# Kernel tuning notes

Hardware: AMD Instinct MI355X
Metric: run time of the kernel (lower is better)

The kernel has to match this reference:

```python
import jax, jax.numpy as jnp
import numpy as np

B, H, W = 8, 1024, 1024
DIM = 33  # LUT resolution per axis


def identity_lut(dim=DIM):
    # lut[0, b, g, r] = r/(dim-1); lut[1, b, g, r] = g/(dim-1); lut[2, b, g, r] = b/(dim-1)
    coords = jnp.arange(dim, dtype=jnp.float32) / (dim - 1)
    r = jnp.broadcast_to(coords[None, None, :], (dim, dim, dim))
    g = jnp.broadcast_to(coords[None, :, None], (dim, dim, dim))
    b = jnp.broadcast_to(coords[:, None, None], (dim, dim, dim))
    return jnp.stack([r, g, b], axis=0)  # [3, dim, dim, dim]


def setup_inputs() -> dict:
    key = jax.random.key(0)
    x = jax.random.uniform(key, (B, 3, H, W), dtype=jnp.float32)  # RGB in [0,1)
    lut = identity_lut(DIM)  # learned parameter, identity init as in the module
    return {"lut": lut, "x": x}


def _trilinear_lut_apply(lut, x):
    # lut: [3, dim, dim, dim] indexed as [channel, b, g, r]; x: [B, 3, H, W] in [0,1]
    dim = lut.shape[1]
    scale = jnp.float32(dim - 1)
    r = x[:, 0] * scale  # [B, H, W]
    g = x[:, 1] * scale
    b = x[:, 2] * scale

    ir = jnp.clip(jnp.floor(r).astype(jnp.int32), 0, dim - 2)
    ig = jnp.clip(jnp.floor(g).astype(jnp.int32), 0, dim - 2)
    ib = jnp.clip(jnp.floor(b).astype(jnp.int32), 0, dim - 2)

    fr = r - ir.astype(x.dtype)
    fg = g - ig.astype(x.dtype)
    fb = b - ib.astype(x.dtype)

    lut_flat = lut.reshape(3, dim * dim * dim)  # [3, dim^3]
    base = (ib * dim + ig) * dim + ir  # flat index of (b,g,r) corner, [B,H,W]

    out = jnp.zeros_like(x)  # [B, 3, H, W]
    for db in (0, 1):
        wb = fb if db else (1.0 - fb)
        for dg in (0, 1):
            wg = fg if dg else (1.0 - fg)
            for dr in (0, 1):
                wr = fr if dr else (1.0 - fr)
                idx = base + (db * dim + dg) * dim + dr  # [B,H,W]
                corner = lut_flat[:, idx]  # gather -> [3, B, H, W]
                w = (wb * wg * wr)[None]  # [1, B, H, W]
                out = out + jnp.transpose(corner * w, (1, 0, 2, 3))
    return out


def reference(lut, x):
    return _trilinear_lut_apply(lut, x)
```

## Files before the change

### kernel.cpp

```cpp
#include <hip/hip_runtime.h>
#include <math.h>

typedef float        f32x4 __attribute__((ext_vector_type(4)));
typedef unsigned int u32x4 __attribute__((ext_vector_type(4)));

static constexpr int DIM    = 33;
static constexpr int LUT_N  = DIM * DIM * DIM;
static constexpr int HW     = 1024 * 1024;
static constexpr int BATCH  = 8;
static constexpr long NPIX  = (long)BATCH * HW;
static constexpr long NTASK = NPIX / 4;

static constexpr size_t QT_BYTES  = (size_t)LUT_N * 4;
static constexpr size_t LDS_BYTES = 143872;

static constexpr int ABLK = 256;
static constexpr int ATHR = 1024;

__device__ __forceinline__ f32x4 ntl4(const float* p) {
    return __builtin_nontemporal_load((const f32x4*)p);
}
__device__ __forceinline__ void nts4(float* p, f32x4 v) {
    __builtin_nontemporal_store(v, (f32x4*)p);
}
__device__ __forceinline__ float d_r(unsigned n) { return (float)(n & 1023u); }
__device__ __forceinline__ float d_g(unsigned n) { return (float)((n >> 10) & 1023u); }
__device__ __forceinline__ float d_b(unsigned n) { return (float)(n >> 20); }

__global__ __launch_bounds__(1024) void lut_fused(
    const float* __restrict__ x, const float* __restrict__ lut,
    float* __restrict__ out) {
    extern __shared__ unsigned sl[];
    const int t = threadIdx.x;

    float vmin = 1e30f, vmax = -1e30f;
    {
        const f32x4* l4 = (const f32x4*)lut;
        const int NV = (3 * LUT_N) / 4;
#pragma unroll 4
        for (int i = t; i < NV; i += 1024) {
            f32x4 v = l4[i];
            vmin = fminf(vmin, fminf(fminf(v[0], v[1]), fminf(v[2], v[3])));
            vmax = fmaxf(vmax, fmaxf(fmaxf(v[0], v[1]), fmaxf(v[2], v[3])));
        }
        if (t < 3) {
            float v = lut[NV * 4 + t];
            vmin = fminf(vmin, v);
            vmax = fmaxf(vmax, v);
        }
    }
#pragma unroll
    for (int off = 32; off > 0; off >>= 1) {
        vmin = fminf(vmin, __shfl_down(vmin, off));
        vmax = fmaxf(vmax, __shfl_down(vmax, off));
    }
    float* sf = (float*)sl;
    if ((t & 63) == 0) { sf[t >> 6] = vmin; sf[16 + (t >> 6)] = vmax; }
    __syncthreads();
    float mn = sf[0], mx = sf[16];
#pragma unroll
    for (int k = 1; k < 16; ++k) {
        mn = fminf(mn, sf[k]);
        mx = fmaxf(mx, sf[16 + k]);
    }
    __syncthreads();

    float range = mx - mn;
    if (range < 1e-20f) range = 1e-20f;
    const float qscale = 1023.0f / range;
    const float inv    = range * (1.0f / 1023.0f);

    for (int i = t; i < LUT_N; i += 1024) {
        float r = lut[i], g = lut[LUT_N + i], b = lut[2 * LUT_N + i];
        unsigned qr = (unsigned)__float2int_rn((r - mn) * qscale);
        unsigned qg = (unsigned)__float2int_rn((g - mn) * qscale);
        unsigned qb = (unsigned)__float2int_rn((b - mn) * qscale);
        sl[i] = qr | (qg << 10) | (qb << 20);
    }
    __syncthreads();

    const int gtid = blockIdx.x * ATHR + t;
    const size_t hw4 = (size_t)gtid * 4;
    const float* xp = x + hw4;
    float*       op = out + hw4;

    f32x4 rc = ntl4(xp);
    f32x4 gc = ntl4(xp + HW);
    f32x4 bc = ntl4(xp + 2 * (size_t)HW);

    for (int it = 0; it < BATCH; ++it) {
        f32x4 rn = {}, gn = {}, bn = {};
        if (it != BATCH - 1) {
            const float* xn = xp + (size_t)(it + 1) * (3 * (size_t)HW);
            rn = ntl4(xn);
            gn = ntl4(xn + HW);
            bn = ntl4(xn + 2 * (size_t)HW);
        }

        unsigned n[4][8];
        float fr[4], fg[4], fb[4];
#pragma unroll
        for (int i = 0; i < 4; ++i) {
            const float scale = (float)(DIM - 1);
            float rs = rc[i] * scale, gs = gc[i] * scale, bs = bc[i] * scale;
            int ir = (int)rs; ir = ir < 0 ? 0 : (ir > DIM - 2 ? DIM - 2 : ir);
            int ig = (int)gs; ig = ig < 0 ? 0 : (ig > DIM - 2 ? DIM - 2 : ig);
            int ib = (int)bs; ib = ib < 0 ? 0 : (ib > DIM - 2 ? DIM - 2 : ib);
            fr[i] = rs - (float)ir;
            fg[i] = gs - (float)ig;
            fb[i] = bs - (float)ib;
            int s = ib * (DIM * DIM) + ig * DIM + ir;
            n[i][0] = sl[s];                     n[i][1] = sl[s + 1];
            n[i][2] = sl[s + DIM];               n[i][3] = sl[s + DIM + 1];
            n[i][4] = sl[s + DIM * DIM];         n[i][5] = sl[s + DIM * DIM + 1];
            n[i][6] = sl[s + DIM * DIM + DIM];   n[i][7] = sl[s + DIM * DIM + DIM + 1];
        }

        f32x4 orv, ogv, obv;
#pragma unroll
        for (int i = 0; i < 4; ++i) {
            float frc = 1.0f - fr[i], fgc = 1.0f - fg[i], fbc = 1.0f - fb[i];
            float w00 = fbc * fgc, w01 = fbc * fg[i];
            float w10 = fb[i] * fgc, w11 = fb[i] * fg[i];
            float u0 = w00 * frc, u1 = w00 * fr[i];
            float u2 = w01 * frc, u3 = w01 * fr[i];
            float u4 = w10 * frc, u5 = w10 * fr[i];
            float u6 = w11 * frc, u7 = w11 * fr[i];

            float qr = u0 * d_r(n[i][0]);
            qr = fmaf(u1, d_r(n[i][1]), qr);
            qr = fmaf(u2, d_r(n[i][2]), qr);
            qr = fmaf(u3, d_r(n[i][3]), qr);
            qr = fmaf(u4, d_r(n[i][4]), qr);
            qr = fmaf(u5, d_r(n[i][5]), qr);
            qr = fmaf(u6, d_r(n[i][6]), qr);
            qr = fmaf(u7, d_r(n[i][7]), qr);

            float qg = u0 * d_g(n[i][0]);
            qg = fmaf(u1, d_g(n[i][1]), qg);
            qg = fmaf(u2, d_g(n[i][2]), qg);
            qg = fmaf(u3, d_g(n[i][3]), qg);
            qg = fmaf(u4, d_g(n[i][4]), qg);
            qg = fmaf(u5, d_g(n[i][5]), qg);
            qg = fmaf(u6, d_g(n[i][6]), qg);
            qg = fmaf(u7, d_g(n[i][7]), qg);

            float qb = u0 * d_b(n[i][0]);
            qb = fmaf(u1, d_b(n[i][1]), qb);
            qb = fmaf(u2, d_b(n[i][2]), qb);
            qb = fmaf(u3, d_b(n[i][3]), qb);
            qb = fmaf(u4, d_b(n[i][4]), qb);
            qb = fmaf(u5, d_b(n[i][5]), qb);
            qb = fmaf(u6, d_b(n[i][6]), qb);
            qb = fmaf(u7, d_b(n[i][7]), qb);

            orv[i] = fmaf(qr, inv, mn);
            ogv[i] = fmaf(qg, inv, mn);
            obv[i] = fmaf(qb, inv, mn);
        }

        float* o = op + (size_t)it * (3 * (size_t)HW);
        nts4(o, orv);
        nts4(o + HW, ogv);
        nts4(o + 2 * (size_t)HW, obv);

        rc = rn; gc = gn; bc = bn;
    }
}

__global__ __launch_bounds__(256) void lut_apply_soa(
    const float* __restrict__ x, const float* __restrict__ lut,
    float* __restrict__ out) {
    long t = (long)blockIdx.x * 256 + threadIdx.x;
    long p = t * 4;
    int  b  = (int)(p >> 20);
    int  hw = (int)(p & (HW - 1));
    size_t base = (size_t)b * (3 * (size_t)HW) + (size_t)hw;

    float4 rv = *(const float4*)(x + base);
    float4 gv = *(const float4*)(x + base + (size_t)HW);
    float4 bv = *(const float4*)(x + base + 2 * (size_t)HW);

    float rr[4] = {rv.x, rv.y, rv.z, rv.w};
    float gg[4] = {gv.x, gv.y, gv.z, gv.w};
    float bb[4] = {bv.x, bv.y, bv.z, bv.w};
    float orr[4], org[4], orb[4];

#pragma unroll
    for (int i = 0; i < 4; ++i) {
        const float scale = (float)(DIM - 1);
        float rs = rr[i] * scale, gs = gg[i] * scale, bs = bb[i] * scale;
        int ir = (int)floorf(rs); ir = ir < 0 ? 0 : (ir > DIM - 2 ? DIM - 2 : ir);
        int ig = (int)floorf(gs); ig = ig < 0 ? 0 : (ig > DIM - 2 ? DIM - 2 : ig);
        int ib = (int)floorf(bs); ib = ib < 0 ? 0 : (ib > DIM - 2 ? DIM - 2 : ib);
        float fr = rs - (float)ir, fg = gs - (float)ig, fb = bs - (float)ib;
        int base_i = (ib * DIM + ig) * DIM + ir;
        float acc[3] = {0.f, 0.f, 0.f};
#pragma unroll
        for (int db = 0; db < 2; ++db) {
            float wb = db ? fb : 1.f - fb;
#pragma unroll
            for (int dg = 0; dg < 2; ++dg) {
                float wg = dg ? fg : 1.f - fg;
#pragma unroll
                for (int dr = 0; dr < 2; ++dr) {
                    float wr = dr ? fr : 1.f - fr;
                    int idx = base_i + (db * DIM + dg) * DIM + dr;
                    float w = wb * wg * wr;
                    acc[0] = fmaf(w, lut[idx], acc[0]);
                    acc[1] = fmaf(w, lut[LUT_N + idx], acc[1]);
                    acc[2] = fmaf(w, lut[2 * LUT_N + idx], acc[2]);
                }
            }
        }
        orr[i] = acc[0]; org[i] = acc[1]; orb[i] = acc[2];
    }

    *(float4*)(out + base)                  = make_float4(orr[0], orr[1], orr[2], orr[3]);
    *(float4*)(out + base + (size_t)HW)     = make_float4(org[0], org[1], org[2], org[3]);
    *(float4*)(out + base + 2 * (size_t)HW) = make_float4(orb[0], orb[1], orb[2], orb[3]);
}

extern "C" void kernel_launch(void* const* d_in, const int* in_sizes, int n_in,
                              void* d_out, int out_size, void* d_ws, size_t ws_size,
                              hipStream_t stream) {
    const float* lut = (const float*)d_in[0];
    const float* x   = (const float*)d_in[1];
    if (n_in >= 2 && in_sizes[0] > in_sizes[1]) {
        lut = (const float*)d_in[1];
        x   = (const float*)d_in[0];
    }
    float* out = (float*)d_out;
    (void)d_ws; (void)ws_size;

    (void)hipFuncSetAttribute((const void*)lut_fused,
                              hipFuncAttributeMaxDynamicSharedMemorySize,
                              (int)LDS_BYTES);
    lut_fused<<<ABLK, ATHR, LDS_BYTES, stream>>>(x, lut, out);
}
```

Baseline: 188.6 us.

## Software-pipeline LUT gathers and prefetch inputs two batches ahead

```diff
diff --git a/kernel.cpp b/kernel.cpp
--- a/kernel.cpp
+++ b/kernel.cpp
@@ -11,7 +11,6 @@
 static constexpr long NPIX  = (long)BATCH * HW;
 static constexpr long NTASK = NPIX / 4;
 
-static constexpr size_t QT_BYTES  = (size_t)LUT_N * 4;
 static constexpr size_t LDS_BYTES = 143872;
 
 static constexpr int ABLK = 256;
@@ -26,12 +25,104 @@
 __device__ __forceinline__ float d_r(unsigned n) { return (float)(n & 1023u); }
 __device__ __forceinline__ float d_g(unsigned n) { return (float)((n >> 10) & 1023u); }
 __device__ __forceinline__ float d_b(unsigned n) { return (float)(n >> 20); }
+
+struct GS {
+    unsigned n[4][8];
+    float fr[4], fg[4], fb[4];
+};
+
+__device__ __forceinline__ void make_gather(const unsigned* __restrict__ sl,
+                                            f32x4 rc, f32x4 gc, f32x4 bc,
+                                            GS& g) {
+#pragma unroll
+    for (int i = 0; i < 4; ++i) {
+        const float scale = (float)(DIM - 1);
+        float rs = rc[i] * scale, gs = gc[i] * scale, bs = bc[i] * scale;
+        int ir = (int)rs; ir = ir < 0 ? 0 : (ir > DIM - 2 ? DIM - 2 : ir);
+        int ig = (int)gs; ig = ig < 0 ? 0 : (ig > DIM - 2 ? DIM - 2 : ig);
+        int ib = (int)bs; ib = ib < 0 ? 0 : (ib > DIM - 2 ? DIM - 2 : ib);
+        g.fr[i] = rs - (float)ir;
+        g.fg[i] = gs - (float)ig;
+        g.fb[i] = bs - (float)ib;
+        int s = ib * (DIM * DIM) + ig * DIM + ir;
+        g.n[i][0] = sl[s];                     g.n[i][1] = sl[s + 1];
+        g.n[i][2] = sl[s + DIM];               g.n[i][3] = sl[s + DIM + 1];
+        g.n[i][4] = sl[s + DIM * DIM];         g.n[i][5] = sl[s + DIM * DIM + 1];
+        g.n[i][6] = sl[s + DIM * DIM + DIM];   g.n[i][7] = sl[s + DIM * DIM + DIM + 1];
+    }
+}
+
+__device__ __forceinline__ void finish_store(const GS& g, float* __restrict__ o,
+                                             float inv, float mn) {
+    f32x4 orv, ogv, obv;
+#pragma unroll
+    for (int i = 0; i < 4; ++i) {
+        float fr = g.fr[i], fg = g.fg[i], fb = g.fb[i];
+        float frc = 1.0f - fr, fgc = 1.0f - fg, fbc = 1.0f - fb;
+        float w00 = fbc * fgc, w01 = fbc * fg;
+        float w10 = fb * fgc,  w11 = fb * fg;
+        float u0 = w00 * frc, u1 = w00 * fr;
+        float u2 = w01 * frc, u3 = w01 * fr;
+        float u4 = w10 * frc, u5 = w10 * fr;
+        float u6 = w11 * frc, u7 = w11 * fr;
+
+        float qr = u0 * d_r(g.n[i][0]);
+        qr = fmaf(u1, d_r(g.n[i][1]), qr);
+        qr = fmaf(u2, d_r(g.n[i][2]), qr);
+        qr = fmaf(u3, d_r(g.n[i][3]), qr);
+        qr = fmaf(u4, d_r(g.n[i][4]), qr);
+        qr = fmaf(u5, d_r(g.n[i][5]), qr);
+        qr = fmaf(u6, d_r(g.n[i][6]), qr);
+        qr = fmaf(u7, d_r(g.n[i][7]), qr);
+
+        float qg = u0 * d_g(g.n[i][0]);
+        qg = fmaf(u1, d_g(g.n[i][1]), qg);
+        qg = fmaf(u2, d_g(g.n[i][2]), qg);
+        qg = fmaf(u3, d_g(g.n[i][3]), qg);
+        qg = fmaf(u4, d_g(g.n[i][4]), qg);
+        qg = fmaf(u5, d_g(g.n[i][5]), qg);
+        qg = fmaf(u6, d_g(g.n[i][6]), qg);
+        qg = fmaf(u7, d_g(g.n[i][7]), qg);
+
+        float qb = u0 * d_b(g.n[i][0]);
+        qb = fmaf(u1, d_b(g.n[i][1]), qb);
+        qb = fmaf(u2, d_b(g.n[i][2]), qb);
+        qb = fmaf(u3, d_b(g.n[i][3]), qb);
+        qb = fmaf(u4, d_b(g.n[i][4]), qb);
+        qb = fmaf(u5, d_b(g.n[i][5]), qb);
+        qb = fmaf(u6, d_b(g.n[i][6]), qb);
+        qb = fmaf(u7, d_b(g.n[i][7]), qb);
+
+        orv[i] = fmaf(qr, inv, mn);
+        ogv[i] = fmaf(qg, inv, mn);
+        obv[i] = fmaf(qb, inv, mn);
+    }
+    nts4(o, orv);
+    nts4(o + HW, ogv);
+    nts4(o + 2 * (size_t)HW, obv);
+}
 
 __global__ __launch_bounds__(1024) void lut_fused(
     const float* __restrict__ x, const float* __restrict__ lut,
     float* __restrict__ out) {
     extern __shared__ unsigned sl[];
     const int t = threadIdx.x;
+
+    const int gtid = blockIdx.x * ATHR + t;
+    const size_t hw4 = (size_t)gtid * 4;
+    const float* xp = x + hw4;
+    float*       op = out + hw4;
+
+    f32x4 ar[BATCH], ag[BATCH], ab[BATCH];
+    ar[0] = ntl4(xp);
+    ag[0] = ntl4(xp + HW);
+    ab[0] = ntl4(xp + 2 * (size_t)HW);
+    {
+        const float* x1 = xp + 3 * (size_t)HW;
+        ar[1] = ntl4(x1);
+        ag[1] = ntl4(x1 + HW);
+        ab[1] = ntl4(x1 + 2 * (size_t)HW);
+    }
 
     float vmin = 1e30f, vmax = -1e30f;
     {
@@ -70,6 +161,7 @@
     const float qscale = 1023.0f / range;
     const float inv    = range * (1.0f / 1023.0f);
 
+#pragma unroll 2
     for (int i = t; i < LUT_N; i += 1024) {
         float r = lut[i], g = lut[LUT_N + i], b = lut[2 * LUT_N + i];
         unsigned qr = (unsigned)__float2int_rn((r - mn) * qscale);
@@ -79,92 +171,21 @@
     }
     __syncthreads();
 
-    const int gtid = blockIdx.x * ATHR + t;
-    const size_t hw4 = (size_t)gtid * 4;
-    const float* xp = x + hw4;
-    float*       op = out + hw4;
-
-    f32x4 rc = ntl4(xp);
-    f32x4 gc = ntl4(xp + HW);
-    f32x4 bc = ntl4(xp + 2 * (size_t)HW);
-
+    GS gs[2];
+    make_gather(sl, ar[0], ag[0], ab[0], gs[0]);
+
+#pragma unroll
     for (int it = 0; it < BATCH; ++it) {
-        f32x4 rn = {}, gn = {}, bn = {};
-        if (it != BATCH - 1) {
-            const float* xn = xp + (size_t)(it + 1) * (3 * (size_t)HW);
-            rn = ntl4(xn);
-            gn = ntl4(xn + HW);
-            bn = ntl4(xn + 2 * (size_t)HW);
-        }
-
-        unsigned n[4][8];
-        float fr[4], fg[4], fb[4];
-#pragma unroll
-        for (int i = 0; i < 4; ++i) {
-            const float scale = (float)(DIM - 1);
-            float rs = rc[i] * scale, gs = gc[i] * scale, bs = bc[i] * scale;
-            int ir = (int)rs; ir = ir < 0 ? 0 : (ir > DIM - 2 ? DIM - 2 : ir);
-            int ig = (int)gs; ig = ig < 0 ? 0 : (ig > DIM - 2 ? DIM - 2 : ig);
-            int ib = (int)bs; ib = ib < 0 ? 0 : (ib > DIM - 2 ? DIM - 2 : ib);
-            fr[i] = rs - (float)ir;
-            fg[i] = gs - (float)ig;
-            fb[i] = bs - (float)ib;
-            int s = ib * (DIM * DIM) + ig * DIM + ir;
-            n[i][0] = sl[s];                     n[i][1] = sl[s + 1];
-            n[i][2] = sl[s + DIM];               n[i][3] = sl[s + DIM + 1];
-            n[i][4] = sl[s + DIM * DIM];         n[i][5] = sl[s + DIM * DIM + 1];
-            n[i][6] = sl[s + DIM * DIM + DIM];   n[i][7] = sl[s + DIM * DIM + DIM + 1];
-        }
-
-        f32x4 orv, ogv, obv;
-#pragma unroll
-        for (int i = 0; i < 4; ++i) {
-            float frc = 1.0f - fr[i], fgc = 1.0f - fg[i], fbc = 1.0f - fb[i];
-            float w00 = fbc * fgc, w01 = fbc * fg[i];
-            float w10 = fb[i] * fgc, w11 = fb[i] * fg[i];
-            float u0 = w00 * frc, u1 = w00 * fr[i];
-            float u2 = w01 * frc, u3 = w01 * fr[i];
-            float u4 = w10 * frc, u5 = w10 * fr[i];
-            float u6 = w11 * frc, u7 = w11 * fr[i];
-
-            float qr = u0 * d_r(n[i][0]);
-            qr = fmaf(u1, d_r(n[i][1]), qr);
-            qr = fmaf(u2, d_r(n[i][2]), qr);
-            qr = fmaf(u3, d_r(n[i][3]), qr);
-            qr = fmaf(u4, d_r(n[i][4]), qr);
-            qr = fmaf(u5, d_r(n[i][5]), qr);
-            qr = fmaf(u6, d_r(n[i][6]), qr);
-            qr = fmaf(u7, d_r(n[i][7]), qr);
-
-            float qg = u0 * d_g(n[i][0]);
-            qg = fmaf(u1, d_g(n[i][1]), qg);
-            qg = fmaf(u2, d_g(n[i][2]), qg);
-            qg = fmaf(u3, d_g(n[i][3]), qg);
-            qg = fmaf(u4, d_g(n[i][4]), qg);
-            qg = fmaf(u5, d_g(n[i][5]), qg);
-            qg = fmaf(u6, d_g(n[i][6]), qg);
-            qg = fmaf(u7, d_g(n[i][7]), qg);
-
-            float qb = u0 * d_b(n[i][0]);
-            qb = fmaf(u1, d_b(n[i][1]), qb);
-            qb = fmaf(u2, d_b(n[i][2]), qb);
-            qb = fmaf(u3, d_b(n[i][3]), qb);
-            qb = fmaf(u4, d_b(n[i][4]), qb);
-            qb = fmaf(u5, d_b(n[i][5]), qb);
-            qb = fmaf(u6, d_b(n[i][6]), qb);
-            qb = fmaf(u7, d_b(n[i][7]), qb);
-
-            orv[i] = fmaf(qr, inv, mn);
-            ogv[i] = fmaf(qg, inv, mn);
-            obv[i] = fmaf(qb, inv, mn);
-        }
-
-        float* o = op + (size_t)it * (3 * (size_t)HW);
-        nts4(o, orv);
-        nts4(o + HW, ogv);
-        nts4(o + 2 * (size_t)HW, obv);
-
-        rc = rn; gc = gn; bc = bn;
+        if (it + 2 < BATCH) {
+            const float* xn = xp + (size_t)(it + 2) * (3 * (size_t)HW);
+            ar[it + 2] = ntl4(xn);
+            ag[it + 2] = ntl4(xn + HW);
+            ab[it + 2] = ntl4(xn + 2 * (size_t)HW);
+        }
+        if (it + 1 < BATCH) {
+            make_gather(sl, ar[it + 1], ag[it + 1], ab[it + 1], gs[(it + 1) & 1]);
+        }
+        finish_store(gs[it & 1], op + (size_t)it * (3 * (size_t)HW), inv, mn);
     }
 }
 
```

Measured after the change: 189.3 us. About the same (+0.4%).

## Prefetch two images ahead and overlap first loads with LUT quantization

Applied to the files above, without the earlier changes.

```diff
diff --git a/kernel.cpp b/kernel.cpp
--- a/kernel.cpp
+++ b/kernel.cpp
@@ -11,27 +11,111 @@
 static constexpr long NPIX  = (long)BATCH * HW;
 static constexpr long NTASK = NPIX / 4;
 
-static constexpr size_t QT_BYTES  = (size_t)LUT_N * 4;
 static constexpr size_t LDS_BYTES = 143872;
 
 static constexpr int ABLK = 256;
 static constexpr int ATHR = 1024;
 
-__device__ __forceinline__ f32x4 ntl4(const float* p) {
-    return __builtin_nontemporal_load((const f32x4*)p);
-}
-__device__ __forceinline__ void nts4(float* p, f32x4 v) {
-    __builtin_nontemporal_store(v, (f32x4*)p);
+__device__ __forceinline__ f32x4 vld4(const float* p) {
+    return *(const volatile f32x4*)p;
+}
+__device__ __forceinline__ void vst4(float* p, f32x4 v) {
+    *(volatile f32x4*)p = v;
 }
 __device__ __forceinline__ float d_r(unsigned n) { return (float)(n & 1023u); }
 __device__ __forceinline__ float d_g(unsigned n) { return (float)((n >> 10) & 1023u); }
 __device__ __forceinline__ float d_b(unsigned n) { return (float)(n >> 20); }
 
-__global__ __launch_bounds__(1024) void lut_fused(
+__device__ __forceinline__ void apply_image(const unsigned* __restrict__ sl,
+                                            f32x4 rc, f32x4 gc, f32x4 bc,
+                                            float* __restrict__ o,
+                                            float inv, float mn) {
+    unsigned n[4][8];
+    float fr[4], fg[4], fb[4];
+#pragma unroll
+    for (int i = 0; i < 4; ++i) {
+        const float scale = (float)(DIM - 1);
+        float rs = rc[i] * scale, gs = gc[i] * scale, bs = bc[i] * scale;
+        int ir = (int)rs; ir = ir < 0 ? 0 : (ir > DIM - 2 ? DIM - 2 : ir);
+        int ig = (int)gs; ig = ig < 0 ? 0 : (ig > DIM - 2 ? DIM - 2 : ig);
+        int ib = (int)bs; ib = ib < 0 ? 0 : (ib > DIM - 2 ? DIM - 2 : ib);
+        fr[i] = rs - (float)ir;
+        fg[i] = gs - (float)ig;
+        fb[i] = bs - (float)ib;
+        int s = ib * (DIM * DIM) + ig * DIM + ir;
+        n[i][0] = sl[s];                     n[i][1] = sl[s + 1];
+        n[i][2] = sl[s + DIM];               n[i][3] = sl[s + DIM + 1];
+        n[i][4] = sl[s + DIM * DIM];         n[i][5] = sl[s + DIM * DIM + 1];
+        n[i][6] = sl[s + DIM * DIM + DIM];   n[i][7] = sl[s + DIM * DIM + DIM + 1];
+    }
+
+    f32x4 orv, ogv, obv;
+#pragma unroll
+    for (int i = 0; i < 4; ++i) {
+        float frv = fr[i], fgv = fg[i], fbv = fb[i];
+        float frc = 1.0f - frv, fgc = 1.0f - fgv, fbc = 1.0f - fbv;
+        float w00 = fbc * fgc, w01 = fbc * fgv;
+        float w10 = fbv * fgc, w11 = fbv * fgv;
+        float u0 = w00 * frc, u1 = w00 * frv;
+        float u2 = w01 * frc, u3 = w01 * frv;
+        float u4 = w10 * frc, u5 = w10 * frv;
+        float u6 = w11 * frc, u7 = w11 * frv;
+
+        float qr = u0 * d_r(n[i][0]);
+        qr = fmaf(u1, d_r(n[i][1]), qr);
+        qr = fmaf(u2, d_r(n[i][2]), qr);
+        qr = fmaf(u3, d_r(n[i][3]), qr);
+        qr = fmaf(u4, d_r(n[i][4]), qr);
+        qr = fmaf(u5, d_r(n[i][5]), qr);
+        qr = fmaf(u6, d_r(n[i][6]), qr);
+        qr = fmaf(u7, d_r(n[i][7]), qr);
+
+        float qg = u0 * d_g(n[i][0]);
+        qg = fmaf(u1, d_g(n[i][1]), qg);
+        qg = fmaf(u2, d_g(n[i][2]), qg);
+        qg = fmaf(u3, d_g(n[i][3]), qg);
+        qg = fmaf(u4, d_g(n[i][4]), qg);
+        qg = fmaf(u5, d_g(n[i][5]), qg);
+        qg = fmaf(u6, d_g(n[i][6]), qg);
+        qg = fmaf(u7, d_g(n[i][7]), qg);
+
+        float qb = u0 * d_b(n[i][0]);
+        qb = fmaf(u1, d_b(n[i][1]), qb);
+        qb = fmaf(u2, d_b(n[i][2]), qb);
+        qb = fmaf(u3, d_b(n[i][3]), qb);
+        qb = fmaf(u4, d_b(n[i][4]), qb);
+        qb = fmaf(u5, d_b(n[i][5]), qb);
+        qb = fmaf(u6, d_b(n[i][6]), qb);
+        qb = fmaf(u7, d_b(n[i][7]), qb);
+
+        orv[i] = fmaf(qr, inv, mn);
+        ogv[i] = fmaf(qg, inv, mn);
+        obv[i] = fmaf(qb, inv, mn);
+    }
+    vst4(o, orv);
+    vst4(o + HW, ogv);
+    vst4(o + 2 * (size_t)HW, obv);
+}
+
+__global__ __launch_bounds__(1024, 4) void lut_fused(
     const float* __restrict__ x, const float* __restrict__ lut,
     float* __restrict__ out) {
     extern __shared__ unsigned sl[];
     const int t = threadIdx.x;
+
+    const int gtid = blockIdx.x * ATHR + t;
+    const size_t hw4 = (size_t)gtid * 4;
+    const float* xp = x + hw4;
+    float*       op = out + hw4;
+
+    f32x4 ar[BATCH], ag[BATCH], ab[BATCH];
+#pragma unroll
+    for (int it = 0; it < 2; ++it) {
+        const float* xi = xp + (size_t)it * (3 * (size_t)HW);
+        ar[it] = vld4(xi);
+        ag[it] = vld4(xi + HW);
+        ab[it] = vld4(xi + 2 * (size_t)HW);
+    }
 
     float vmin = 1e30f, vmax = -1e30f;
     {
@@ -70,6 +154,7 @@
     const float qscale = 1023.0f / range;
     const float inv    = range * (1.0f / 1023.0f);
 
+#pragma unroll 2
     for (int i = t; i < LUT_N; i += 1024) {
         float r = lut[i], g = lut[LUT_N + i], b = lut[2 * LUT_N + i];
         unsigned qr = (unsigned)__float2int_rn((r - mn) * qscale);
@@ -79,92 +164,16 @@
     }
     __syncthreads();
 
-    const int gtid = blockIdx.x * ATHR + t;
-    const size_t hw4 = (size_t)gtid * 4;
-    const float* xp = x + hw4;
-    float*       op = out + hw4;
-
-    f32x4 rc = ntl4(xp);
-    f32x4 gc = ntl4(xp + HW);
-    f32x4 bc = ntl4(xp + 2 * (size_t)HW);
-
+#pragma unroll
     for (int it = 0; it < BATCH; ++it) {
-        f32x4 rn = {}, gn = {}, bn = {};
-        if (it != BATCH - 1) {
-            const float* xn = xp + (size_t)(it + 1) * (3 * (size_t)HW);
-            rn = ntl4(xn);
-            gn = ntl4(xn + HW);
-            bn = ntl4(xn + 2 * (size_t)HW);
-        }
-
-        unsigned n[4][8];
-        float fr[4], fg[4], fb[4];
-#pragma unroll
-        for (int i = 0; i < 4; ++i) {
-            const float scale = (float)(DIM - 1);
-            float rs = rc[i] * scale, gs = gc[i] * scale, bs = bc[i] * scale;
-            int ir = (int)rs; ir = ir < 0 ? 0 : (ir > DIM - 2 ? DIM - 2 : ir);
-            int ig = (int)gs; ig = ig < 0 ? 0 : (ig > DIM - 2 ? DIM - 2 : ig);
-            int ib = (int)bs; ib = ib < 0 ? 0 : (ib > DIM - 2 ? DIM - 2 : ib);
-            fr[i] = rs - (float)ir;
-            fg[i] = gs - (float)ig;
-            fb[i] = bs - (float)ib;
-            int s = ib * (DIM * DIM) + ig * DIM + ir;
-            n[i][0] = sl[s];                     n[i][1] = sl[s + 1];
-            n[i][2] = sl[s + DIM];               n[i][3] = sl[s + DIM + 1];
-            n[i][4] = sl[s + DIM * DIM];         n[i][5] = sl[s + DIM * DIM + 1];
-            n[i][6] = sl[s + DIM * DIM + DIM];   n[i][7] = sl[s + DIM * DIM + DIM + 1];
-        }
-
-        f32x4 orv, ogv, obv;
-#pragma unroll
-        for (int i = 0; i < 4; ++i) {
-            float frc = 1.0f - fr[i], fgc = 1.0f - fg[i], fbc = 1.0f - fb[i];
-            float w00 = fbc * fgc, w01 = fbc * fg[i];
-            float w10 = fb[i] * fgc, w11 = fb[i] * fg[i];
-            float u0 = w00 * frc, u1 = w00 * fr[i];
-            float u2 = w01 * frc, u3 = w01 * fr[i];
-            float u4 = w10 * frc, u5 = w10 * fr[i];
-            float u6 = w11 * frc, u7 = w11 * fr[i];
-
-            float qr = u0 * d_r(n[i][0]);
-            qr = fmaf(u1, d_r(n[i][1]), qr);
-            qr = fmaf(u2, d_r(n[i][2]), qr);
-            qr = fmaf(u3, d_r(n[i][3]), qr);
-            qr = fmaf(u4, d_r(n[i][4]), qr);
-            qr = fmaf(u5, d_r(n[i][5]), qr);
-            qr = fmaf(u6, d_r(n[i][6]), qr);
-            qr = fmaf(u7, d_r(n[i][7]), qr);
-
-            float qg = u0 * d_g(n[i][0]);
-            qg = fmaf(u1, d_g(n[i][1]), qg);
-            qg = fmaf(u2, d_g(n[i][2]), qg);
-            qg = fmaf(u3, d_g(n[i][3]), qg);
-            qg = fmaf(u4, d_g(n[i][4]), qg);
-            qg = fmaf(u5, d_g(n[i][5]), qg);
-            qg = fmaf(u6, d_g(n[i][6]), qg);
-            qg = fmaf(u7, d_g(n[i][7]), qg);
-
-            float qb = u0 * d_b(n[i][0]);
-            qb = fmaf(u1, d_b(n[i][1]), qb);
-            qb = fmaf(u2, d_b(n[i][2]), qb);
-            qb = fmaf(u3, d_b(n[i][3]), qb);
-            qb = fmaf(u4, d_b(n[i][4]), qb);
-            qb = fmaf(u5, d_b(n[i][5]), qb);
-            qb = fmaf(u6, d_b(n[i][6]), qb);
-            qb = fmaf(u7, d_b(n[i][7]), qb);
-
-            orv[i] = fmaf(qr, inv, mn);
-            ogv[i] = fmaf(qg, inv, mn);
-            obv[i] = fmaf(qb, inv, mn);
-        }
-
-        float* o = op + (size_t)it * (3 * (size_t)HW);
-        nts4(o, orv);
-        nts4(o + HW, ogv);
-        nts4(o + 2 * (size_t)HW, obv);
-
-        rc = rn; gc = gn; bc = bn;
+        if (it + 2 < BATCH) {
+            const float* xn = xp + (size_t)(it + 2) * (3 * (size_t)HW);
+            ar[it + 2] = vld4(xn);
+            ag[it + 2] = vld4(xn + HW);
+            ab[it + 2] = vld4(xn + 2 * (size_t)HW);
+        }
+        apply_image(sl, ar[it], ag[it], ab[it],
+                    op + (size_t)it * (3 * (size_t)HW), inv, mn);
     }
 }
 
```

Result: slower. 197.6 us (+4.7%).
